# Performance work log

Measured on AMD Instinct MI355X. Metric: run time of the kernel, lower is better.

The kernel has to match this reference:

```python
import math
import jax, jax.numpy as jnp
import numpy as np

EPS = 1e-6  # router.key_norm.eps
TEMPERATURE = 1.0  # router.temperature


def _rms_norm_base(x, eps=EPS):
    # matches torch _rms_norm_base: fp32 RMS normalization WITHOUT weight
    x = x.astype(jnp.float32)
    inv = jax.lax.rsqrt(jnp.mean(x * x, axis=-1, keepdims=True) + eps)
    return x * inv


def setup_inputs() -> dict:
    key = jax.random.key(0)
    k1, k2, k3, k4 = jax.random.split(key, 4)
    n, b, t, d = 6, 2, 4096, 1024
    return {
        "blocks": jax.random.normal(k1, (n, b, t, d), jnp.float32),
        "partial_block": jax.random.normal(k2, (b, t, d), jnp.float32),
        "w_query": jax.random.normal(k3, (d,), jnp.float32),
        "norm_weight": jax.random.normal(k4, (d,), jnp.float32),
    }


def reference(blocks, partial_block, w_query, norm_weight):
    # blocks: [n, b, t, d] completed block states; partial_block: [b, t, d]
    d = blocks.shape[-1]
    scale = math.sqrt(d) * TEMPERATURE
    # _router_effective_query: w_query * key_norm.weight, in fp32
    query = (w_query.astype(jnp.float32) * norm_weight.astype(jnp.float32))

    # ---- attend_completed_blocks (phase 1) ----
    sources = jnp.moveaxis(blocks, 0, 2)                      # [b, t, n, d]
    base_keys = _rms_norm_base(sources)                       # fp32
    scores = jnp.einsum('d,btnd->btn', query, base_keys) / scale
    p1_max = jnp.max(scores, axis=-1)                         # [b, t]
    shifted = scores - p1_max[..., None]
    exp_s = jnp.exp(shifted)
    p1_lse = jnp.sum(exp_s, axis=-1)                          # [b, t]
    # unnormalized weighted sum (lse folded into merge weights below)
    routed = jnp.einsum('btn,btnd->btd', exp_s, sources.astype(jnp.float32))
    probs = exp_s / p1_lse[..., None]
    log_probs = shifted - jnp.log(p1_lse)[..., None]
    p1_entropy = -jnp.sum(probs * log_probs, axis=-1)         # [b, t]

    # ---- merge_with_partial_block (online-softmax merge) ----
    partial_scores = jnp.einsum('d,btd->bt', query, _rms_norm_base(partial_block)) / scale
    merged_max = jnp.maximum(p1_max, partial_scores)
    phase1_coeff = jnp.exp(p1_max - merged_max)
    partial_coeff = jnp.exp(partial_scores - merged_max)
    denom = phase1_coeff * p1_lse + partial_coeff
    phase1_weight = phase1_coeff * p1_lse / denom             # [b, t]
    partial_weight = partial_coeff / denom                    # [b, t]
    hidden = routed * phase1_weight[..., None] + partial_block * partial_weight[..., None]

    w1 = jnp.maximum(phase1_weight, 1e-8)
    wp = jnp.maximum(partial_weight, 1e-8)
    entropy = w1 * p1_entropy - w1 * jnp.log(w1) - wp * jnp.log(wp)
    return hidden, entropy
```

## Files before the change

kernel.cpp:

```cpp
#include <hip/hip_runtime.h>
#include <math.h>


#define D 1024
#define NBLK 6
#define C4 4

typedef float vf4 __attribute__((ext_vector_type(4)));

__global__ __launch_bounds__(256) void reskip_router_kernel(
    const float* __restrict__ blocks,
    const float* __restrict__ partial,
    const float* __restrict__ w_query,
    const float* __restrict__ norm_w,
    float* __restrict__ out_hidden,
    float* __restrict__ out_entropy,
    int BT)
{
    const int wave = threadIdx.x >> 6;
    const int lane = threadIdx.x & 63;
    const int tok  = blockIdx.x * 4 + wave;
    if (tok >= BT) return;

    const float inv_d     = 1.0f / (float)D;
    const float inv_scale = 1.0f / 32.0f;
    const float eps       = 1e-6f;

    const size_t tokOff    = (size_t)tok * D;
    const size_t blkStride = (size_t)BT * D;

    vf4 v[NBLK + 1][C4];
#pragma unroll
    for (int i = 0; i < NBLK; ++i) {
        const vf4* p = (const vf4*)(blocks + (size_t)i * blkStride + tokOff);
#pragma unroll
        for (int c = 0; c < C4; ++c)
            v[i][c] = __builtin_nontemporal_load(&p[c * 64 + lane]);
    }
    {
        const vf4* p = (const vf4*)(partial + tokOff);
#pragma unroll
        for (int c = 0; c < C4; ++c)
            v[NBLK][c] = __builtin_nontemporal_load(&p[c * 64 + lane]);
    }

    const vf4* wq4 = (const vf4*)w_query;
    const vf4* nw4 = (const vf4*)norm_w;
    vf4 q[C4];
#pragma unroll
    for (int c = 0; c < C4; ++c)
        q[c] = wq4[c * 64 + lane] * nw4[c * 64 + lane];

    float ss[NBLK + 1], dt[NBLK + 1];
#pragma unroll
    for (int i = 0; i <= NBLK; ++i) {
        float s = 0.0f, d = 0.0f;
#pragma unroll
        for (int c = 0; c < C4; ++c) {
            vf4 x = v[i][c];
            s += x.x * x.x + x.y * x.y + x.z * x.z + x.w * x.w;
            d += q[c].x * x.x + q[c].y * x.y + q[c].z * x.z + q[c].w * x.w;
        }
        ss[i] = s; dt[i] = d;
    }

#pragma unroll
    for (int off = 32; off > 0; off >>= 1) {
#pragma unroll
        for (int i = 0; i <= NBLK; ++i) {
            ss[i] += __shfl_xor(ss[i], off, 64);
            dt[i] += __shfl_xor(dt[i], off, 64);
        }
    }

    float sc[NBLK + 1];
#pragma unroll
    for (int i = 0; i <= NBLK; ++i)
        sc[i] = dt[i] * rsqrtf(ss[i] * inv_d + eps) * inv_scale;

    float M6 = sc[0];
#pragma unroll
    for (int i = 1; i < NBLK; ++i) M6 = fmaxf(M6, sc[i]);

    float e[NBLK], l = 0.0f, T = 0.0f;
#pragma unroll
    for (int i = 0; i < NBLK; ++i) {
        float sh = sc[i] - M6;
        e[i] = expf(sh);
        l += e[i];
        T += e[i] * sh;
    }
    float p1_ent = logf(l) - T / l;

    float psc   = sc[NBLK];
    float mm    = fmaxf(M6, psc);
    float c1    = expf(M6 - mm);
    float cp    = expf(psc - mm);
    float denom = c1 * l + cp;
    float w1    = c1 * l / denom;
    float wp    = cp / denom;

    vf4* outp = (vf4*)(out_hidden + tokOff);
#pragma unroll
    for (int c = 0; c < C4; ++c) {
        vf4 acc = v[NBLK][c] * wp;
#pragma unroll
        for (int i = 0; i < NBLK; ++i)
            acc += v[i][c] * (e[i] * w1);
        __builtin_nontemporal_store(acc, &outp[c * 64 + lane]);
    }

    if (lane == 0) {
        float w1c = fmaxf(w1, 1e-8f);
        float wpc = fmaxf(wp, 1e-8f);
        out_entropy[tok] = w1c * p1_ent - w1c * logf(w1c) - wpc * logf(wpc);
    }
}

extern "C" void kernel_launch(void* const* d_in, const int* in_sizes, int n_in,
                              void* d_out, int out_size, void* d_ws, size_t ws_size,
                              hipStream_t stream) {
    const float* blocks  = (const float*)d_in[0];
    const float* partial = (const float*)d_in[1];
    const float* wq      = (const float*)d_in[2];
    const float* nw      = (const float*)d_in[3];
    float* out = (float*)d_out;

    const int BT = in_sizes[1] / D;
    float* out_hidden  = out;
    float* out_entropy = out + (size_t)BT * D;

    const int grid = (BT + 3) / 4;
    reskip_router_kernel<<<grid, 256, 0, stream>>>(
        blocks, partial, wq, nw, out_hidden, out_entropy, BT);
}
```

Baseline: 286.9 us.

## Assign one token per workgroup with cross-wave LDS reduction

Moves from one wave per token, where each lane held 4 vec4 per source, to one 256-thread workgroup per token, where each thread holds a single vec4 per source. Per-wave shuffle sums are combined across the four waves through shared memory and a barrier. This cuts register pressure per thread (7 vec4 instead of 28) so more waves can be resident to hide memory latency, at the cost of a __syncthreads, an LDS round trip and four times as many workgroups.

After: 295.0 us. 1.03x slower.

```diff
diff --git a/kernel.cpp b/kernel.cpp
--- a/kernel.cpp
+++ b/kernel.cpp
@@ -4,7 +4,6 @@
 
 #define D 1024
 #define NBLK 6
-#define C4 4
 
 typedef float vf4 __attribute__((ext_vector_type(4)));
 
@@ -17,10 +16,10 @@
     float* __restrict__ out_entropy,
     int BT)
 {
-    const int wave = threadIdx.x >> 6;
-    const int lane = threadIdx.x & 63;
-    const int tok  = blockIdx.x * 4 + wave;
-    if (tok >= BT) return;
+    const int tid  = threadIdx.x;
+    const int lane = tid & 63;
+    const int wv   = tid >> 6;
+    const int tok  = blockIdx.x;
 
     const float inv_d     = 1.0f / (float)D;
     const float inv_scale = 1.0f / 32.0f;
@@ -29,39 +28,22 @@
     const size_t tokOff    = (size_t)tok * D;
     const size_t blkStride = (size_t)BT * D;
 
-    vf4 v[NBLK + 1][C4];
+    vf4 v[NBLK + 1];
 #pragma unroll
     for (int i = 0; i < NBLK; ++i) {
         const vf4* p = (const vf4*)(blocks + (size_t)i * blkStride + tokOff);
-#pragma unroll
-        for (int c = 0; c < C4; ++c)
-            v[i][c] = __builtin_nontemporal_load(&p[c * 64 + lane]);
+        v[i] = __builtin_nontemporal_load(&p[tid]);
     }
-    {
-        const vf4* p = (const vf4*)(partial + tokOff);
-#pragma unroll
-        for (int c = 0; c < C4; ++c)
-            v[NBLK][c] = __builtin_nontemporal_load(&p[c * 64 + lane]);
-    }
+    v[NBLK] = __builtin_nontemporal_load(&((const vf4*)(partial + tokOff))[tid]);
 
-    const vf4* wq4 = (const vf4*)w_query;
-    const vf4* nw4 = (const vf4*)norm_w;
-    vf4 q[C4];
-#pragma unroll
-    for (int c = 0; c < C4; ++c)
-        q[c] = wq4[c * 64 + lane] * nw4[c * 64 + lane];
+    vf4 q = ((const vf4*)w_query)[tid] * ((const vf4*)norm_w)[tid];
 
     float ss[NBLK + 1], dt[NBLK + 1];
 #pragma unroll
     for (int i = 0; i <= NBLK; ++i) {
-        float s = 0.0f, d = 0.0f;
-#pragma unroll
-        for (int c = 0; c < C4; ++c) {
-            vf4 x = v[i][c];
-            s += x.x * x.x + x.y * x.y + x.z * x.z + x.w * x.w;
-            d += q[c].x * x.x + q[c].y * x.y + q[c].z * x.z + q[c].w * x.w;
-        }
-        ss[i] = s; dt[i] = d;
+        vf4 x = v[i];
+        ss[i] = x.x * x.x + x.y * x.y + x.z * x.z + x.w * x.w;
+        dt[i] = q.x * x.x + q.y * x.y + q.z * x.z + q.w * x.w;
     }
 
 #pragma unroll
@@ -71,6 +53,21 @@
             ss[i] += __shfl_xor(ss[i], off, 64);
             dt[i] += __shfl_xor(dt[i], off, 64);
         }
+    }
+
+    __shared__ float red[4][2][NBLK + 1];
+    if (lane == 0) {
+#pragma unroll
+        for (int i = 0; i <= NBLK; ++i) {
+            red[wv][0][i] = ss[i];
+            red[wv][1][i] = dt[i];
+        }
+    }
+    __syncthreads();
+#pragma unroll
+    for (int i = 0; i <= NBLK; ++i) {
+        ss[i] = red[0][0][i] + red[1][0][i] + red[2][0][i] + red[3][0][i];
+        dt[i] = red[0][1][i] + red[1][1][i] + red[2][1][i] + red[3][1][i];
     }
 
     float sc[NBLK + 1];
@@ -100,17 +97,13 @@
     float w1    = c1 * l / denom;
     float wp    = cp / denom;
 
-    vf4* outp = (vf4*)(out_hidden + tokOff);
+    vf4 acc = v[NBLK] * wp;
 #pragma unroll
-    for (int c = 0; c < C4; ++c) {
-        vf4 acc = v[NBLK][c] * wp;
-#pragma unroll
-        for (int i = 0; i < NBLK; ++i)
-            acc += v[i][c] * (e[i] * w1);
-        __builtin_nontemporal_store(acc, &outp[c * 64 + lane]);
-    }
+    for (int i = 0; i < NBLK; ++i)
+        acc += v[i] * (e[i] * w1);
+    __builtin_nontemporal_store(acc, &((vf4*)(out_hidden + tokOff))[tid]);
 
-    if (lane == 0) {
+    if (tid == 0) {
         float w1c = fmaxf(w1, 1e-8f);
         float wpc = fmaxf(wp, 1e-8f);
         out_entropy[tok] = w1c * p1_ent - w1c * logf(w1c) - wpc * logf(wpc);
@@ -130,7 +123,6 @@
     float* out_hidden  = out;
     float* out_entropy = out + (size_t)BT * D;
 
-    const int grid = (BT + 3) / 4;
-    reskip_router_kernel<<<grid, 256, 0, stream>>>(
+    reskip_router_kernel<<<BT, 256, 0, stream>>>(
         blocks, partial, wq, nw, out_hidden, out_entropy, BT);
 }
```
